# Kernel tuning notes

Hardware: AMD Instinct MI355X
Metric: run time of the kernel (lower is better)

The kernel has to match this reference:

```python
import jax, jax.numpy as jnp
import numpy as np

NUM_IN = 1024
HIDDEN = 32  # pooling_hidden_dim fixed in PoolingFunction
N = 200000


def setup_inputs() -> dict:
    key = jax.random.key(0)
    ks = jax.random.split(key, 7)
    s_in = 1.0 / np.sqrt(NUM_IN)
    s_h = 1.0 / np.sqrt(HIDDEN)
    return {
        "x": jax.random.normal(ks[0], (N, NUM_IN), dtype=jnp.float32),
        "V_w": jax.random.uniform(ks[1], (HIDDEN, NUM_IN), jnp.float32, -s_in, s_in),
        "V_b": jax.random.uniform(ks[2], (HIDDEN,), jnp.float32, -s_in, s_in),
        "U_w": jax.random.uniform(ks[3], (HIDDEN, NUM_IN), jnp.float32, -s_in, s_in),
        "U_b": jax.random.uniform(ks[4], (HIDDEN,), jnp.float32, -s_in, s_in),
        "w_w": jax.random.uniform(ks[5], (1, HIDDEN), jnp.float32, -s_h, s_h),
        "w_b": jax.random.uniform(ks[6], (1,), jnp.float32, -s_h, s_h),
    }


def reference(x, V_w, V_b, U_w, U_b, w_w, w_b):
    # x: [N, num_in]
    a_v = jnp.tanh(x @ V_w.T + V_b)          # [N, H]
    a_u = jax.nn.sigmoid(x @ U_w.T + U_b)    # [N, H]
    a = (a_v * a_u) @ w_w.T + w_b            # [N, 1] attention logits
    a = jax.nn.softmax(a.T, axis=1)          # [1, N]
    m = a @ x                                # [1, num_in]
    return m
```

## Files before the change

kernel.cpp:

```cpp
#include <hip/hip_runtime.h>
#include <math.h>

#define NUM_IN 1024
#define TILE_R 16
#define NB_MAX 256
#define PR_OSTRIDE 17
#define PR_QSTRIDE (64 * PR_OSTRIDE + 4)

using bf16x8 = __attribute__((ext_vector_type(8))) short;
using f32x4  = __attribute__((ext_vector_type(4))) float;

__device__ __forceinline__ unsigned int f2bf1(float f) {
  unsigned int u = __float_as_uint(f);
  return (u + 0x7fffu + ((u >> 16) & 1u)) >> 16;
}
__device__ __forceinline__ unsigned int pk2(float a, float b) {
  return f2bf1(a) | (f2bf1(b) << 16);
}
__device__ __forceinline__ float bf2f(unsigned int s) {
  return __uint_as_float(s << 16);
}

#define BARX() do { \
  __builtin_amdgcn_sched_barrier(0); \
  asm volatile("s_waitcnt lgkmcnt(0)" ::: "memory"); \
  __builtin_amdgcn_s_barrier(); \
  __builtin_amdgcn_sched_barrier(0); \
} while (0)

#define WAIT_VM0() do { \
  __builtin_amdgcn_sched_barrier(0); \
  asm volatile("s_waitcnt vmcnt(0)" ::: "memory"); \
  __builtin_amdgcn_sched_barrier(0); \
} while (0)

__global__ __launch_bounds__(512, 1) void ga_main(
    const float* __restrict__ x,
    const float* __restrict__ Vw, const float* __restrict__ Uw,
    const float* __restrict__ Vb, const float* __restrict__ Ub,
    const float* __restrict__ ww, const float* __restrict__ wb,
    float* __restrict__ wsAcc, float* __restrict__ wsM, float* __restrict__ wsS,
    int nb, int nTiles)
{
  __shared__ __align__(16) unsigned short xbuf[2][TILE_R * NUM_IN];
  __shared__ __align__(16) float prered[8 * PR_QSTRIDE];
  __shared__ __align__(16) float lgs[TILE_R];

  const int tid = threadIdx.x;
  const int b   = blockIdx.x;
  const int w   = tid >> 6;
  const int l   = tid & 63;
  const int l15 = l & 15;
  const int kg  = l >> 4;
  const int h   = tid & 31;
  const int rr  = tid >> 5;

  const float vbh = Vb[h], ubh = Ub[h], wwh = ww[h];
  const float wb0 = wb[0];

  uint4 bfr[4][4];
  {
    #pragma unroll
    for (int nt = 0; nt < 4; ++nt) {
      const int o = (nt << 4) + l15;
      const float* Wr = (o < 32) ? (Vw + (size_t)o * NUM_IN) : (Uw + (size_t)(o - 32) * NUM_IN);
      #pragma unroll
      for (int s = 0; s < 4; ++s) {
        const int k0 = (w << 7) + (s << 5) + (kg << 3);
        const float4 a = *reinterpret_cast<const float4*>(Wr + k0);
        const float4 c = *reinterpret_cast<const float4*>(Wr + k0 + 4);
        uint4 v;
        v.x = pk2(a.x, a.y); v.y = pk2(a.z, a.w);
        v.z = pk2(c.x, c.y); v.w = pk2(c.z, c.w);
        bfr[nt][s] = v;
      }
    }
    #pragma unroll
    for (int nt = 0; nt < 4; ++nt)
      #pragma unroll
      for (int s = 0; s < 4; ++s)
        asm volatile("" : "+v"(bfr[nt][s].x), "+v"(bfr[nt][s].y),
                          "+v"(bfr[nt][s].z), "+v"(bfr[nt][s].w));
  }

  const char* xb8 = (const char*)x;
  const int inRow = (w << 9) + (kg << 5);

  float4 sA[4], sB[4];
  uint4  xf[4];

  #define ISSUE(Tt) do { \
    const char* base_ = xb8 + ((size_t)(Tt) * TILE_R + l15) * 4096 + inRow; \
    sA[0] = *reinterpret_cast<const float4*>(base_      );  sB[0] = *reinterpret_cast<const float4*>(base_ +  16); \
    sA[1] = *reinterpret_cast<const float4*>(base_ + 128);  sB[1] = *reinterpret_cast<const float4*>(base_ + 144); \
    sA[2] = *reinterpret_cast<const float4*>(base_ + 256);  sB[2] = *reinterpret_cast<const float4*>(base_ + 272); \
    sA[3] = *reinterpret_cast<const float4*>(base_ + 384);  sB[3] = *reinterpret_cast<const float4*>(base_ + 400); \
  } while (0)

  #define CONVERT(bufidx) do { \
    char* dst_ = (char*)&xbuf[bufidx][0] + (l15 << 11); \
    _Pragma("unroll") \
    for (int s = 0; s < 4; ++s) { \
      uint4 v_; \
      v_.x = pk2(sA[s].x, sA[s].y); v_.y = pk2(sA[s].z, sA[s].w); \
      v_.z = pk2(sB[s].x, sB[s].y); v_.w = pk2(sB[s].z, sB[s].w); \
      xf[s] = v_; \
      const int cb_ = ((w << 8) + (s << 6) + (kg << 4)) ^ ((l15 & 7) << 4); \
      *reinterpret_cast<uint4*>(dst_ + cb_) = v_; \
    } \
    _Pragma("unroll") \
    for (int s = 0; s < 4; ++s) \
      asm volatile("" : "+v"(xf[s].x), "+v"(xf[s].y), "+v"(xf[s].z), "+v"(xf[s].w)); \
  } while (0)

  float M = -INFINITY, S = 0.f;
  float aX = 0.f, aY = 0.f;
  int cur = 0;
  int T = b;

  ISSUE(T);
  WAIT_VM0();
  CONVERT(0);
  if (T + nb < nTiles) ISSUE(T + nb);
  BARX();

  while (true) {
    const bool more1 = (T + nb)     < nTiles;
    const bool more2 = (T + 2 * nb) < nTiles;

    {
      f32x4 acc[4] = {{0.f,0.f,0.f,0.f},{0.f,0.f,0.f,0.f},{0.f,0.f,0.f,0.f},{0.f,0.f,0.f,0.f}};
      #pragma unroll
      for (int s = 0; s < 4; ++s) {
        const bf16x8 af = __builtin_bit_cast(bf16x8, xf[s]);
        #pragma unroll
        for (int nt = 0; nt < 4; ++nt)
          acc[nt] = __builtin_amdgcn_mfma_f32_16x16x32_bf16(
              af, __builtin_bit_cast(bf16x8, bfr[nt][s]), acc[nt], 0, 0, 0);
      }
      #pragma unroll
      for (int nt = 0; nt < 4; ++nt) {
        const int obase = w * PR_QSTRIDE + ((nt << 4) + l15) * PR_OSTRIDE + (kg << 2);
        #pragma unroll
        for (int r = 0; r < 4; ++r) prered[obase + r] = acc[nt][r];
      }
    }
    BARX();

    if (more1) {
      WAIT_VM0();
      CONVERT(cur ^ 1);
      if (more2) ISSUE(T + 2 * nb);
    }
    {
      float pv = vbh, pu = ubh;
      #pragma unroll
      for (int q = 0; q < 8; ++q) {
        pv += prered[q * PR_QSTRIDE + h * PR_OSTRIDE + rr];
        pu += prered[q * PR_QSTRIDE + (h + 32) * PR_OSTRIDE + rr];
      }
      const float ev = __expf(2.f * pv);
      const float av = (ev - 1.f) * __builtin_amdgcn_rcpf(ev + 1.f);
      const float au = __builtin_amdgcn_rcpf(1.f + __expf(-pu));
      float g = av * au * wwh;
      g += __shfl_xor(g, 1);
      g += __shfl_xor(g, 2);
      g += __shfl_xor(g, 4);
      g += __shfl_xor(g, 8);
      g += __shfl_xor(g, 16);
      if (h == 0) lgs[rr] = g + wb0;
    }
    BARX();

    {
      float lf[16];
      #pragma unroll
      for (int j = 0; j < 16; ++j) lf[j] = lgs[j];
      float mc = lf[0];
      #pragma unroll
      for (int j = 1; j < 16; ++j) mc = fmaxf(mc, lf[j]);
      const float newM = fmaxf(M, mc);
      const float scale = __expf(M - newM);
      S *= scale; aX *= scale; aY *= scale;
      const char* xbsrc = (const char*)&xbuf[cur][0];
      #pragma unroll
      for (int j = 0; j < 16; ++j) {
        const float p = __expf(lf[j] - newM);
        S += p;
        const unsigned int xv = *reinterpret_cast<const unsigned int*>(
            xbsrc + (j << 11) + (((tid << 2)) ^ ((j & 7) << 4)));
        aX += p * bf2f(xv & 0xffffu);
        aY += p * bf2f(xv >> 16);
      }
      M = newM;
    }
    BARX();

    if (!more1) break;
    cur ^= 1;
    T += nb;
  }

  *reinterpret_cast<float2*>(&wsAcc[(size_t)b * NUM_IN + (tid << 1)]) = make_float2(aX, aY);
  if (tid == 0) { wsM[b] = M; wsS[b] = S; }
}

__global__ void ga_reduceMS(const float* __restrict__ wsM, const float* __restrict__ wsS,
                            float* __restrict__ wsW, float* __restrict__ wsT, int nb)
{
  __shared__ float sm[8], ss[8];
  const int t = threadIdx.x;
  float m = (t < nb) ? wsM[t] : -INFINITY;
  float mm = m;
  #pragma unroll
  for (int d = 1; d < 64; d <<= 1) mm = fmaxf(mm, __shfl_xor(mm, d));
  if ((t & 63) == 0) sm[t >> 6] = mm;
  __syncthreads();
  const float M = fmaxf(fmaxf(fmaxf(sm[0], sm[1]), fmaxf(sm[2], sm[3])),
                        fmaxf(fmaxf(sm[4], sm[5]), fmaxf(sm[6], sm[7])));
  const float wg = (t < nb) ? __expf(m - M) : 0.f;
  if (t < nb) wsW[t] = wg;
  float s = wg * ((t < nb) ? wsS[t] : 0.f);
  #pragma unroll
  for (int d = 1; d < 64; d <<= 1) s += __shfl_xor(s, d);
  if ((t & 63) == 0) ss[t >> 6] = s;
  __syncthreads();
  if (t == 0) {
    float St = 0.f;
    #pragma unroll
    for (int k = 0; k < 8; ++k) St += ss[k];
    wsT[0] = St;
  }
}

__global__ void ga_combine(const float* __restrict__ wsAcc, const float* __restrict__ wsW,
                           const float* __restrict__ wsT, float* __restrict__ out, int nb)
{
  __shared__ float red[8][32];
  const int t = threadIdx.x;
  const int col = (blockIdx.x << 5) + (t & 31);
  const int seg = t >> 5;
  float s = 0.f;
  for (int ii = 0; ii < 64; ++ii) {
    const int i = (seg << 6) + ii;
    if (i < nb) s = fmaf(wsW[i], wsAcc[(size_t)i * NUM_IN + col], s);
  }
  red[seg][t & 31] = s;
  __syncthreads();
  if (seg == 0) {
    float tot = 0.f;
    #pragma unroll
    for (int k = 0; k < 8; ++k) tot += red[k][t];
    out[col] = tot / wsT[0];
  }
}

extern "C" void kernel_launch(void* const* d_in, const int* in_sizes, int n_in,
                              void* d_out, int out_size, void* d_ws, size_t ws_size,
                              hipStream_t stream)
{
  const float* x  = (const float*)d_in[0];
  const float* Vw = (const float*)d_in[1];
  const float* Vb = (const float*)d_in[2];
  const float* Uw = (const float*)d_in[3];
  const float* Ub = (const float*)d_in[4];
  const float* ww = (const float*)d_in[5];
  const float* wb = (const float*)d_in[6];
  float* out = (float*)d_out;

  const int Nrows  = in_sizes[0] / NUM_IN;
  const int nTiles = Nrows / TILE_R;

  const size_t per = (size_t)NUM_IN * 4 + 16;
  int nb = (int)((ws_size - 64) / per);
  if (nb > NB_MAX)  nb = NB_MAX;
  if (nb > nTiles)  nb = nTiles;
  if (nb < 1)       nb = 1;

  float* wsAcc = (float*)d_ws;
  float* wsM   = wsAcc + (size_t)nb * NUM_IN;
  float* wsS   = wsM + nb;
  float* wsW   = wsS + nb;
  float* wsT   = wsW + nb;

  ga_main<<<nb, 512, 0, stream>>>(x, Vw, Uw, Vb, Ub, ww, wb, wsAcc, wsM, wsS, nb, nTiles);
  ga_reduceMS<<<1, 512, 0, stream>>>(wsM, wsS, wsW, wsT, nb);
  ga_combine<<<32, 256, 0, stream>>>(wsAcc, wsW, wsT, out, nb);
}
```

Baseline: 190.0 us.

## Accumulate softmax-weighted x in registers instead of staging tiles in LDS

```diff
diff --git a/kernel.cpp b/kernel.cpp
--- a/kernel.cpp
+++ b/kernel.cpp
@@ -17,9 +17,8 @@
 __device__ __forceinline__ unsigned int pk2(float a, float b) {
   return f2bf1(a) | (f2bf1(b) << 16);
 }
-__device__ __forceinline__ float bf2f(unsigned int s) {
-  return __uint_as_float(s << 16);
-}
+__device__ __forceinline__ float bflo(unsigned int w) { return __uint_as_float(w << 16); }
+__device__ __forceinline__ float bfhi(unsigned int w) { return __uint_as_float(w & 0xffff0000u); }
 
 #define BARX() do { \
   __builtin_amdgcn_sched_barrier(0); \
@@ -42,7 +41,6 @@
     float* __restrict__ wsAcc, float* __restrict__ wsM, float* __restrict__ wsS,
     int nb, int nTiles)
 {
-  __shared__ __align__(16) unsigned short xbuf[2][TILE_R * NUM_IN];
   __shared__ __align__(16) float prered[8 * PR_QSTRIDE];
   __shared__ __align__(16) float lgs[TILE_R];
 
@@ -97,16 +95,11 @@
     sA[3] = *reinterpret_cast<const float4*>(base_ + 384);  sB[3] = *reinterpret_cast<const float4*>(base_ + 400); \
   } while (0)
 
-  #define CONVERT(bufidx) do { \
-    char* dst_ = (char*)&xbuf[bufidx][0] + (l15 << 11); \
+  #define PACK() do { \
     _Pragma("unroll") \
     for (int s = 0; s < 4; ++s) { \
-      uint4 v_; \
-      v_.x = pk2(sA[s].x, sA[s].y); v_.y = pk2(sA[s].z, sA[s].w); \
-      v_.z = pk2(sB[s].x, sB[s].y); v_.w = pk2(sB[s].z, sB[s].w); \
-      xf[s] = v_; \
-      const int cb_ = ((w << 8) + (s << 6) + (kg << 4)) ^ ((l15 & 7) << 4); \
-      *reinterpret_cast<uint4*>(dst_ + cb_) = v_; \
+      xf[s].x = pk2(sA[s].x, sA[s].y); xf[s].y = pk2(sA[s].z, sA[s].w); \
+      xf[s].z = pk2(sB[s].x, sB[s].y); xf[s].w = pk2(sB[s].z, sB[s].w); \
     } \
     _Pragma("unroll") \
     for (int s = 0; s < 4; ++s) \
@@ -114,44 +107,42 @@
   } while (0)
 
   float M = -INFINITY, S = 0.f;
-  float aX = 0.f, aY = 0.f;
-  int cur = 0;
+  float acc[4][8];
+  #pragma unroll
+  for (int s = 0; s < 4; ++s)
+    #pragma unroll
+    for (int i = 0; i < 8; ++i) acc[s][i] = 0.f;
+
   int T = b;
 
   ISSUE(T);
   WAIT_VM0();
-  CONVERT(0);
+  PACK();
   if (T + nb < nTiles) ISSUE(T + nb);
-  BARX();
 
   while (true) {
     const bool more1 = (T + nb)     < nTiles;
     const bool more2 = (T + 2 * nb) < nTiles;
 
     {
-      f32x4 acc[4] = {{0.f,0.f,0.f,0.f},{0.f,0.f,0.f,0.f},{0.f,0.f,0.f,0.f},{0.f,0.f,0.f,0.f}};
+      f32x4 a4[4] = {{0.f,0.f,0.f,0.f},{0.f,0.f,0.f,0.f},{0.f,0.f,0.f,0.f},{0.f,0.f,0.f,0.f}};
       #pragma unroll
       for (int s = 0; s < 4; ++s) {
         const bf16x8 af = __builtin_bit_cast(bf16x8, xf[s]);
         #pragma unroll
         for (int nt = 0; nt < 4; ++nt)
-          acc[nt] = __builtin_amdgcn_mfma_f32_16x16x32_bf16(
-              af, __builtin_bit_cast(bf16x8, bfr[nt][s]), acc[nt], 0, 0, 0);
+          a4[nt] = __builtin_amdgcn_mfma_f32_16x16x32_bf16(
+              af, __builtin_bit_cast(bf16x8, bfr[nt][s]), a4[nt], 0, 0, 0);
       }
       #pragma unroll
       for (int nt = 0; nt < 4; ++nt) {
         const int obase = w * PR_QSTRIDE + ((nt << 4) + l15) * PR_OSTRIDE + (kg << 2);
         #pragma unroll
-        for (int r = 0; r < 4; ++r) prered[obase + r] = acc[nt][r];
+        for (int r = 0; r < 4; ++r) prered[obase + r] = a4[nt][r];
       }
     }
     BARX();
 
-    if (more1) {
-      WAIT_VM0();
-      CONVERT(cur ^ 1);
-      if (more2) ISSUE(T + 2 * nb);
-    }
     {
       float pv = vbh, pu = ubh;
       #pragma unroll
@@ -173,35 +164,61 @@
     BARX();
 
     {
-      float lf[16];
-      #pragma unroll
-      for (int j = 0; j < 16; ++j) lf[j] = lgs[j];
-      float mc = lf[0];
-      #pragma unroll
-      for (int j = 1; j < 16; ++j) mc = fmaxf(mc, lf[j]);
-      const float newM = fmaxf(M, mc);
-      const float scale = __expf(M - newM);
-      S *= scale; aX *= scale; aY *= scale;
-      const char* xbsrc = (const char*)&xbuf[cur][0];
-      #pragma unroll
-      for (int j = 0; j < 16; ++j) {
-        const float p = __expf(lf[j] - newM);
-        S += p;
-        const unsigned int xv = *reinterpret_cast<const unsigned int*>(
-            xbsrc + (j << 11) + (((tid << 2)) ^ ((j & 7) << 4)));
-        aX += p * bf2f(xv & 0xffffu);
-        aY += p * bf2f(xv >> 16);
-      }
-      M = newM;
-    }
-    BARX();
+      const float lf = lgs[l15];
+      float mc = lf;
+      mc = fmaxf(mc, __shfl_xor(mc, 1));
+      mc = fmaxf(mc, __shfl_xor(mc, 2));
+      mc = fmaxf(mc, __shfl_xor(mc, 4));
+      mc = fmaxf(mc, __shfl_xor(mc, 8));
+      if (mc > M) {
+        const float scale = __expf(M - mc);
+        S *= scale;
+        #pragma unroll
+        for (int s = 0; s < 4; ++s)
+          #pragma unroll
+          for (int i = 0; i < 8; ++i) acc[s][i] *= scale;
+        M = mc;
+      }
+      const float p = __expf(lf - M);
+      S += p;
+      #pragma unroll
+      for (int s = 0; s < 4; ++s) {
+        acc[s][0] = fmaf(p, bflo(xf[s].x), acc[s][0]);
+        acc[s][1] = fmaf(p, bfhi(xf[s].x), acc[s][1]);
+        acc[s][2] = fmaf(p, bflo(xf[s].y), acc[s][2]);
+        acc[s][3] = fmaf(p, bfhi(xf[s].y), acc[s][3]);
+        acc[s][4] = fmaf(p, bflo(xf[s].z), acc[s][4]);
+        acc[s][5] = fmaf(p, bfhi(xf[s].z), acc[s][5]);
+        acc[s][6] = fmaf(p, bflo(xf[s].w), acc[s][6]);
+        acc[s][7] = fmaf(p, bfhi(xf[s].w), acc[s][7]);
+      }
+      if (more1) {
+        WAIT_VM0();
+        PACK();
+        if (more2) ISSUE(T + 2 * nb);
+      }
+    }
 
     if (!more1) break;
-    cur ^= 1;
     T += nb;
   }
 
-  *reinterpret_cast<float2*>(&wsAcc[(size_t)b * NUM_IN + (tid << 1)]) = make_float2(aX, aY);
+  #pragma unroll
+  for (int d = 1; d < 16; d <<= 1) {
+    #pragma unroll
+    for (int s = 0; s < 4; ++s)
+      #pragma unroll
+      for (int i = 0; i < 8; ++i) acc[s][i] += __shfl_xor(acc[s][i], d);
+    S += __shfl_xor(S, d);
+  }
+  if (l15 == 0) {
+    #pragma unroll
+    for (int s = 0; s < 4; ++s) {
+      float* dst = &wsAcc[(size_t)b * NUM_IN + (w << 7) + (s << 5) + (kg << 3)];
+      *reinterpret_cast<float4*>(dst)     = make_float4(acc[s][0], acc[s][1], acc[s][2], acc[s][3]);
+      *reinterpret_cast<float4*>(dst + 4) = make_float4(acc[s][4], acc[s][5], acc[s][6], acc[s][7]);
+    }
+  }
   if (tid == 0) { wsM[b] = M; wsS[b] = S; }
 }
 
```

Measured after the change: 180.5 us. 1.05x faster.
